# Kernel optimization log

Measured on AMD Instinct MI355X. Metric: run time of the kernel, lower is better.

Reference implementation:

```python
import jax, jax.numpy as jnp
import numpy as np

N = 20000
E_RAND = 320000
NEG_SLOPE = 0.2


def setup_inputs() -> dict:
    key = jax.random.key(0)
    ks = jax.random.split(key, 10)
    x = jax.random.normal(ks[0], (N, 768), dtype=jnp.float32)
    src = jax.random.randint(ks[1], (E_RAND,), 0, N)
    dst = jax.random.randint(ks[2], (E_RAND,), 0, N)
    loop = jnp.arange(N)
    edge_index = jnp.stack([jnp.concatenate([src, loop]),
                            jnp.concatenate([dst, loop])])  # [2, 340000]
    s = 1.0 / np.sqrt(768.0)
    W1 = jax.random.normal(ks[3], (768, 768), dtype=jnp.float32) * s
    a_src1 = jax.random.normal(ks[4], (8, 96), dtype=jnp.float32) * 0.1
    a_dst1 = jax.random.normal(ks[5], (8, 96), dtype=jnp.float32) * 0.1
    b1 = jnp.zeros((768,), dtype=jnp.float32)
    W2 = jax.random.normal(ks[6], (768, 768), dtype=jnp.float32) * s
    a_src2 = jax.random.normal(ks[7], (1, 768), dtype=jnp.float32) * 0.1
    a_dst2 = jax.random.normal(ks[8], (1, 768), dtype=jnp.float32) * 0.1
    b2 = jnp.zeros((768,), dtype=jnp.float32)
    return {"x": x, "edge_index": edge_index, "W1": W1, "a_src1": a_src1,
            "a_dst1": a_dst1, "b1": b1, "W2": W2, "a_src2": a_src2,
            "a_dst2": a_dst2, "b2": b2}


def gat_layer(x, W, a_src, a_dst, bias, src, dst, heads, out_c, concat):
    n = x.shape[0]
    h = (x @ W).reshape(n, heads, out_c)                      # [N,H,C]
    al_s = jnp.einsum('nhc,hc->nh', h, a_src)                 # [N,H]
    al_d = jnp.einsum('nhc,hc->nh', h, a_dst)
    e = jax.nn.leaky_relu(al_s[src] + al_d[dst], NEG_SLOPE)   # [E,H]
    m = jax.ops.segment_max(e, dst, num_segments=n)           # segment softmax
    ex = jnp.exp(e - m[dst])
    z = jax.ops.segment_sum(ex, dst, num_segments=n)
    alpha = ex / (z[dst] + 1e-16)                             # [E,H]
    msg = h[src] * alpha[:, :, None]                          # [E,H,C]
    out = jax.ops.segment_sum(msg, dst, num_segments=n)       # [N,H,C]
    out = out.reshape(n, heads * out_c) if concat else out.mean(axis=1)
    return out + bias


def reference(x, edge_index, W1, a_src1, a_dst1, b1, W2, a_src2, a_dst2, b2):
    src, dst = edge_index[0], edge_index[1]
    h = gat_layer(x, W1, a_src1, a_dst1, b1, src, dst, heads=8, out_c=96, concat=True)
    h = jax.nn.elu(h)
    out = gat_layer(h, W2, a_src2, a_dst2, b2, src, dst, heads=1, out_c=768, concat=False)
    return out
```

## Files before the change

kernel.cpp:

```cpp
#include <hip/hip_runtime.h>
#include <cstdint>
#include <cstddef>

typedef _Float16 f16;
typedef _Float16 f16x4 __attribute__((ext_vector_type(4)));
typedef _Float16 f16x8 __attribute__((ext_vector_type(8)));
typedef float f32x4 __attribute__((ext_vector_type(4)));

#define LRELU_SLOPE 0.2f

#define GLL16(g, l)                                                          \
  __builtin_amdgcn_global_load_lds(                                          \
      (const __attribute__((address_space(1))) void*)(g),                    \
      (__attribute__((address_space(3))) void*)(l), 16, 0, 0)

__global__ __launch_bounds__(256) void k_prep_xh(const float* __restrict__ x,
                                                 f16* __restrict__ xh,
                                                 int nvalid, int npad) {
  int total = npad * 192;
  for (int idx = blockIdx.x * blockDim.x + threadIdx.x; idx < total;
       idx += gridDim.x * blockDim.x) {
    int row = idx / 192;
    f16x4 o;
    if (row < nvalid) {
      const float4 v = *(const float4*)(x + (size_t)idx * 4);
      o[0] = (f16)v.x; o[1] = (f16)v.y; o[2] = (f16)v.z; o[3] = (f16)v.w;
    } else {
      o[0] = (f16)0.f; o[1] = (f16)0.f; o[2] = (f16)0.f; o[3] = (f16)0.f;
    }
    *(f16x4*)(xh + (size_t)idx * 4) = o;
  }
}

__global__ __launch_bounds__(256) void k_transpose_w(const float* __restrict__ W,
                                                     f16* __restrict__ Wt) {
  __shared__ float tile[32][33];
  int bn = blockIdx.x * 32;
  int bk = blockIdx.y * 32;
  int tx = threadIdx.x & 31, ty = threadIdx.x >> 5;
  #pragma unroll
  for (int r = ty; r < 32; r += 8)
    tile[r][tx] = W[(size_t)(bk + r) * 768 + bn + tx];
  __syncthreads();
  #pragma unroll
  for (int r = ty; r < 32; r += 8)
    Wt[(size_t)(bn + r) * 768 + bk + tx] = (f16)tile[tx][r];
}

__global__ void k_zero_ints(int* __restrict__ p, int n) {
  for (int i = blockIdx.x * blockDim.x + threadIdx.x; i < n;
       i += gridDim.x * blockDim.x) p[i] = 0;
}

__global__ void k_hist(const int* __restrict__ dst, int E, int* __restrict__ counts) {
  for (int e = blockIdx.x * blockDim.x + threadIdx.x; e < E;
       e += gridDim.x * blockDim.x) atomicAdd(&counts[dst[e]], 1);
}

__global__ __launch_bounds__(1024) void k_scan_block(const int* __restrict__ counts,
                                                     int* __restrict__ starts,
                                                     int* __restrict__ cursor, int n) {
  const int t = threadIdx.x;
  const int nthr = 1024;
  const int chunk = (n + nthr - 1) / nthr;
  const int base = t * chunk;
  int tsum = 0;
  for (int i = 0; i < chunk; i++) {
    int idx = base + i;
    if (idx < n) tsum += counts[idx];
  }
  int lane = t & 63, wv = t >> 6;
  int s = tsum;
  #pragma unroll
  for (int off = 1; off < 64; off <<= 1) {
    int tmp = __shfl_up(s, off);
    if (lane >= off) s += tmp;
  }
  __shared__ int wsum[16];
  if (lane == 63) wsum[wv] = s;
  __syncthreads();
  int woff = 0;
  for (int w = 0; w < wv; w++) woff += wsum[w];
  int run = woff + s - tsum;
  for (int i = 0; i < chunk; i++) {
    int idx = base + i;
    if (idx < n) {
      starts[idx] = run;
      cursor[idx] = run;
      run += counts[idx];
    }
  }
  if (t == nthr - 1) starts[n] = run;
}

__global__ void k_fill(const int* __restrict__ src, const int* __restrict__ dst, int E,
                       int* __restrict__ cursor, int* __restrict__ src_sorted) {
  for (int e = blockIdx.x * blockDim.x + threadIdx.x; e < E;
       e += gridDim.x * blockDim.x) {
    int slot = atomicAdd(&cursor[dst[e]], 1);
    src_sorted[slot] = src[e];
  }
}

__global__ __launch_bounds__(256) void k_gemm_f16(const f16* __restrict__ A,
                                                  const f16* __restrict__ Bt,
                                                  f16* __restrict__ C, int Mvalid) {
  __shared__ __align__(16) f16 As[4096];
  __shared__ __align__(16) f16 Bs[4096];
  const int K = 768;
  const int tid = threadIdx.x;
  const int bm = blockIdx.x * 128;
  const int bn = blockIdx.y * 128;
  const int lane = tid & 63;
  const int wave = tid >> 6;
  const int wr = (wave >> 1) * 64;
  const int wc = (wave & 1) * 64;

  const int r0 = tid >> 2;
  const int kc = (tid & 3) ^ ((r0 >> 1) & 3);
  const size_t offA0 = (size_t)(bm + r0) * K + kc * 8;
  const size_t offB0 = (size_t)(bn + r0) * K + kc * 8;
  f16* ldsA0 = As + wave * 512;
  f16* ldsA1 = As + 2048 + wave * 512;
  f16* ldsB0 = Bs + wave * 512;
  f16* ldsB1 = Bs + 2048 + wave * 512;

  f32x4 acc[4][4];
  const f32x4 vzero = {0.f, 0.f, 0.f, 0.f};
  #pragma unroll
  for (int i = 0; i < 4; i++)
    #pragma unroll
    for (int j = 0; j < 4; j++) acc[i][j] = vzero;

  const int fr = lane & 15;
  const int fq = lane >> 4;

  for (int k0 = 0; k0 < K; k0 += 32) {
    GLL16(A + offA0 + k0, ldsA0);
    GLL16(A + offA0 + (size_t)64 * K + k0, ldsA1);
    GLL16(Bt + offB0 + k0, ldsB0);
    GLL16(Bt + offB0 + (size_t)64 * K + k0, ldsB1);
    __syncthreads();
    f16x8 af[4], bf[4];
    #pragma unroll
    for (int i = 0; i < 4; i++) {
      const int r = wr + i * 16 + fr;
      const int slot = fq ^ ((r >> 1) & 3);
      af[i] = *(const f16x8*)(&As[r * 32 + slot * 8]);
    }
    #pragma unroll
    for (int j = 0; j < 4; j++) {
      const int r = wc + j * 16 + fr;
      const int slot = fq ^ ((r >> 1) & 3);
      bf[j] = *(const f16x8*)(&Bs[r * 32 + slot * 8]);
    }
    #pragma unroll
    for (int i = 0; i < 4; i++)
      #pragma unroll
      for (int j = 0; j < 4; j++)
        acc[i][j] = __builtin_amdgcn_mfma_f32_16x16x32_f16(af[i], bf[j], acc[i][j], 0, 0, 0);
    __syncthreads();
  }

  #pragma unroll
  for (int i = 0; i < 4; i++) {
    #pragma unroll
    for (int j = 0; j < 4; j++) {
      const int col = bn + wc + j * 16 + fr;
      #pragma unroll
      for (int r = 0; r < 4; r++) {
        const int row = bm + wr + i * 16 + fq * 4 + r;
        if (row < Mvalid) C[(size_t)row * 768 + col] = (f16)acc[i][j][r];
      }
    }
  }
}

template <int H>
__global__ __launch_bounds__(256) void k_al(const f16* __restrict__ h,
                                            const float* __restrict__ a_src,
                                            const float* __restrict__ a_dst,
                                            float* __restrict__ als,
                                            float* __restrict__ ald, int N) {
  int node = blockIdx.x * 4 + (threadIdx.x >> 6);
  int lane = threadIdx.x & 63;
  if (node >= N) return;
  const f16x4* hp = (const f16x4*)(h + (size_t)node * 768 + lane * 12);
  float ss = 0.f, sd = 0.f;
  int cbase = lane * 12;
  #pragma unroll
  for (int q = 0; q < 3; q++) {
    f16x4 hv = hp[q];
    #pragma unroll
    for (int j = 0; j < 4; j++) {
      int c = cbase + q * 4 + j;
      float v = (float)hv[j];
      ss += v * a_src[c];
      sd += v * a_dst[c];
    }
  }
  const int red = (H == 8) ? 8 : 64;
  #pragma unroll
  for (int off = 1; off < red; off <<= 1) {
    ss += __shfl_xor(ss, off);
    sd += __shfl_xor(sd, off);
  }
  if (H == 8) {
    if ((lane & 7) == 0) {
      als[(size_t)node * 8 + (lane >> 3)] = ss;
      ald[(size_t)node * 8 + (lane >> 3)] = sd;
    }
  } else {
    if (lane == 0) { als[node] = ss; ald[node] = sd; }
  }
}

template <int H, bool FINAL>
__global__ __launch_bounds__(192) void k_aggregate(
    const f16* __restrict__ h, const float* __restrict__ als,
    const float* __restrict__ ald, const int* __restrict__ starts,
    const int* __restrict__ src_sorted, const float* __restrict__ bias,
    void* __restrict__ outv, int nvalid) {
  const int n = blockIdx.x;
  const int t = threadIdx.x;
  if (n >= nvalid) return;
  __shared__ float s_ex[256 * H];
  __shared__ int s_src[256];
  __shared__ float s_zp[3][H];
  const int start = starts[n];
  const int deg = starts[n + 1] - start;
  const int lane = t & 63, wv = t >> 6;
  const int hA = (H == 8) ? (t & 7) : 0;
  const int myh = (H == 8) ? (t / 24) : 0;
  const float ald_A = ald[(size_t)n * H + hA];

  float zpart = 0.f;
  float4 acc = {0.f, 0.f, 0.f, 0.f};

  for (int cb = 0; cb < deg; cb += 256) {
    const int cnt = min(256, deg - cb);
    for (int idx = t; idx < cnt * H; idx += 192) {
      const int e = (H == 8) ? (idx >> 3) : idx;
      const int s = src_sorted[start + cb + e];
      if (H == 1 || (idx & 7) == 0) s_src[e] = s;
      float v = als[(size_t)s * H + hA] + ald_A;
      v = v > 0.f ? v : LRELU_SLOPE * v;
      const float ex = __expf(v);
      s_ex[idx] = ex;
      zpart += ex;
    }
    __syncthreads();
    for (int e = 0; e < cnt; e++) {
      const f16x4 hv = *(const f16x4*)(h + (size_t)s_src[e] * 768 + 4 * t);
      const float a = s_ex[e * H + myh];
      acc.x += a * (float)hv[0];
      acc.y += a * (float)hv[1];
      acc.z += a * (float)hv[2];
      acc.w += a * (float)hv[3];
    }
    __syncthreads();
  }

  if (H == 8) {
    #pragma unroll
    for (int off = 8; off < 64; off <<= 1) zpart += __shfl_xor(zpart, off);
    if (lane < 8) s_zp[wv][lane] = zpart;
  } else {
    #pragma unroll
    for (int off = 1; off < 64; off <<= 1) zpart += __shfl_xor(zpart, off);
    if (lane == 0) s_zp[wv][0] = zpart;
  }
  __syncthreads();
  const float z = s_zp[0][myh] + s_zp[1][myh] + s_zp[2][myh];
  const float inv = 1.f / (z + 1e-16f);

  const float4 bv = *(const float4*)(bias + 4 * t);
  float v0 = acc.x * inv + bv.x;
  float v1 = acc.y * inv + bv.y;
  float v2 = acc.z * inv + bv.z;
  float v3 = acc.w * inv + bv.w;
  if (!FINAL) {
    v0 = v0 > 0.f ? v0 : expm1f(v0);
    v1 = v1 > 0.f ? v1 : expm1f(v1);
    v2 = v2 > 0.f ? v2 : expm1f(v2);
    v3 = v3 > 0.f ? v3 : expm1f(v3);
    f16x4 o;
    o[0] = (f16)v0; o[1] = (f16)v1; o[2] = (f16)v2; o[3] = (f16)v3;
    *(f16x4*)((f16*)outv + (size_t)n * 768 + 4 * t) = o;
  } else {
    float4 o = {v0, v1, v2, v3};
    *(float4*)((float*)outv + (size_t)n * 768 + 4 * t) = o;
  }
}

extern "C" void kernel_launch(void* const* d_in, const int* in_sizes, int n_in,
                              void* d_out, int out_size, void* d_ws, size_t ws_size,
                              hipStream_t stream) {
  const float* x   = (const float*)d_in[0];
  const int*   ei  = (const int*)d_in[1];
  const float* W1  = (const float*)d_in[2];
  const float* as1 = (const float*)d_in[3];
  const float* ad1 = (const float*)d_in[4];
  const float* b1  = (const float*)d_in[5];
  const float* W2  = (const float*)d_in[6];
  const float* as2 = (const float*)d_in[7];
  const float* ad2 = (const float*)d_in[8];
  const float* b2  = (const float*)d_in[9];

  const int N = in_sizes[0] / 768;
  const int E = in_sizes[1] / 2;
  const int Mpad = (N + 127) & ~127;
  const int* srcp = ei;
  const int* dstp = ei + E;

  char* p = (char*)d_ws;
  auto alloc = [&](size_t b) { char* r = p; p += (b + 255) & ~(size_t)255; return r; };
  f16*   bufX   = (f16*)alloc((size_t)Mpad * 768 * sizeof(f16));
  f16*   bufH   = (f16*)alloc((size_t)Mpad * 768 * sizeof(f16));
  f16*   Wt1    = (f16*)alloc((size_t)768 * 768 * sizeof(f16));
  f16*   Wt2    = (f16*)alloc((size_t)768 * 768 * sizeof(f16));
  float* als1   = (float*)alloc((size_t)N * 8 * sizeof(float));
  float* ald1   = (float*)alloc((size_t)N * 8 * sizeof(float));
  float* als2   = (float*)alloc((size_t)N * sizeof(float));
  float* ald2   = (float*)alloc((size_t)N * sizeof(float));
  int*   counts = (int*)alloc((size_t)N * sizeof(int));
  int*   starts = (int*)alloc(((size_t)N + 1) * sizeof(int));
  int*   cursor = (int*)alloc((size_t)N * sizeof(int));
  int*   srcs   = (int*)alloc((size_t)E * sizeof(int));

  k_zero_ints<<<dim3(80), dim3(256), 0, stream>>>(counts, N);
  k_hist<<<dim3(512), dim3(256), 0, stream>>>(dstp, E, counts);
  k_scan_block<<<dim3(1), dim3(1024), 0, stream>>>(counts, starts, cursor, N);
  k_fill<<<dim3(512), dim3(256), 0, stream>>>(srcp, dstp, E, cursor, srcs);

  k_prep_xh<<<dim3(1024), dim3(256), 0, stream>>>(x, bufX, N, Mpad);
  k_transpose_w<<<dim3(24, 24), dim3(256), 0, stream>>>(W1, Wt1);
  k_transpose_w<<<dim3(24, 24), dim3(256), 0, stream>>>(W2, Wt2);

  k_gemm_f16<<<dim3(Mpad / 128, 6), dim3(256), 0, stream>>>(bufX, Wt1, bufH, N);
  k_al<8><<<dim3((N + 3) / 4), dim3(256), 0, stream>>>(bufH, as1, ad1, als1, ald1, N);
  k_aggregate<8, false><<<dim3(N), dim3(192), 0, stream>>>(bufH, als1, ald1, starts, srcs, b1, bufX, N);

  k_gemm_f16<<<dim3(Mpad / 128, 6), dim3(256), 0, stream>>>(bufX, Wt2, bufH, N);
  k_al<1><<<dim3((N + 3) / 4), dim3(256), 0, stream>>>(bufH, as2, ad2, als2, ald2, N);
  k_aggregate<1, true><<<dim3(N), dim3(192), 0, stream>>>(bufH, als2, ald2, starts, srcs, b2, d_out, N);
}
```

Baseline: 351.5 us.

## Slice h into 96-column planes and split aggregation per slice with precomputed edge weights

```diff
diff --git a/kernel.cpp b/kernel.cpp
--- a/kernel.cpp
+++ b/kernel.cpp
@@ -94,17 +94,20 @@
 }
 
 __global__ void k_fill(const int* __restrict__ src, const int* __restrict__ dst, int E,
-                       int* __restrict__ cursor, int* __restrict__ src_sorted) {
+                       int* __restrict__ cursor, int* __restrict__ src_sorted,
+                       int* __restrict__ dst_sorted) {
   for (int e = blockIdx.x * blockDim.x + threadIdx.x; e < E;
        e += gridDim.x * blockDim.x) {
     int slot = atomicAdd(&cursor[dst[e]], 1);
     src_sorted[slot] = src[e];
+    dst_sorted[slot] = dst[e];
   }
 }
 
 __global__ __launch_bounds__(256) void k_gemm_f16(const f16* __restrict__ A,
                                                   const f16* __restrict__ Bt,
-                                                  f16* __restrict__ C, int Mvalid) {
+                                                  f16* __restrict__ C, int Mvalid,
+                                                  int SS) {
   __shared__ __align__(16) f16 As[4096];
   __shared__ __align__(16) f16 Bs[4096];
   const int K = 768;
@@ -167,30 +170,34 @@
     #pragma unroll
     for (int j = 0; j < 4; j++) {
       const int col = bn + wc + j * 16 + fr;
+      const int cs = col / 96;
+      const int cw = col - cs * 96;
+      f16* cp = C + (size_t)cs * SS + cw;
       #pragma unroll
       for (int r = 0; r < 4; r++) {
         const int row = bm + wr + i * 16 + fq * 4 + r;
-        if (row < Mvalid) C[(size_t)row * 768 + col] = (f16)acc[i][j][r];
+        if (row < Mvalid) cp[(size_t)row * 96] = (f16)acc[i][j][r];
       }
     }
   }
 }
 
 template <int H>
-__global__ __launch_bounds__(256) void k_al(const f16* __restrict__ h,
+__global__ __launch_bounds__(256) void k_al(const f16* __restrict__ hs,
                                             const float* __restrict__ a_src,
                                             const float* __restrict__ a_dst,
                                             float* __restrict__ als,
-                                            float* __restrict__ ald, int N) {
+                                            float* __restrict__ ald, int N, int SS) {
   int node = blockIdx.x * 4 + (threadIdx.x >> 6);
   int lane = threadIdx.x & 63;
   if (node >= N) return;
-  const f16x4* hp = (const f16x4*)(h + (size_t)node * 768 + lane * 12);
+  const int sl = lane >> 3, wl = lane & 7;
+  const f16* hp = hs + (size_t)sl * SS + (size_t)node * 96 + wl * 12;
   float ss = 0.f, sd = 0.f;
-  int cbase = lane * 12;
+  const int cbase = sl * 96 + wl * 12;
   #pragma unroll
   for (int q = 0; q < 3; q++) {
-    f16x4 hv = hp[q];
+    f16x4 hv = *(const f16x4*)(hp + q * 4);
     #pragma unroll
     for (int j = 0; j < 4; j++) {
       int c = cbase + q * 4 + j;
@@ -207,89 +214,83 @@
   }
   if (H == 8) {
     if ((lane & 7) == 0) {
-      als[(size_t)node * 8 + (lane >> 3)] = ss;
-      ald[(size_t)node * 8 + (lane >> 3)] = sd;
+      als[(size_t)node * 8 + sl] = ss;
+      ald[(size_t)node * 8 + sl] = sd;
     }
   } else {
     if (lane == 0) { als[node] = ss; ald[node] = sd; }
   }
 }
 
+template <int H>
+__global__ __launch_bounds__(256) void k_alpha(const float* __restrict__ als,
+                                               const float* __restrict__ ald,
+                                               const int* __restrict__ srcs,
+                                               const int* __restrict__ dsts,
+                                               float* __restrict__ ex, int E) {
+  const int e = blockIdx.x * 256 + threadIdx.x;
+  if (e >= E) return;
+  const int s = srcs[e], d = dsts[e];
+  #pragma unroll
+  for (int h = 0; h < H; h++) {
+    float v = als[(size_t)s * H + h] + ald[(size_t)d * H + h];
+    v = v > 0.f ? v : LRELU_SLOPE * v;
+    ex[(size_t)h * E + e] = __expf(v);
+  }
+}
+
 template <int H, bool FINAL>
-__global__ __launch_bounds__(192) void k_aggregate(
-    const f16* __restrict__ h, const float* __restrict__ als,
-    const float* __restrict__ ald, const int* __restrict__ starts,
-    const int* __restrict__ src_sorted, const float* __restrict__ bias,
-    void* __restrict__ outv, int nvalid) {
-  const int n = blockIdx.x;
+__global__ __launch_bounds__(192) void k_agg2(
+    const f16* __restrict__ hs, const float* __restrict__ ex,
+    const int* __restrict__ starts, const int* __restrict__ srcs,
+    const float* __restrict__ bias, void* __restrict__ outv,
+    int N, int SS, int E) {
+  const int s = blockIdx.x & 7;
+  const int n = blockIdx.x >> 3;
   const int t = threadIdx.x;
-  if (n >= nvalid) return;
-  __shared__ float s_ex[256 * H];
-  __shared__ int s_src[256];
-  __shared__ float s_zp[3][H];
+  const int k = t / 24;
+  const int c = t - k * 24;
+  const int head = (H == 8) ? s : 0;
   const int start = starts[n];
   const int deg = starts[n + 1] - start;
-  const int lane = t & 63, wv = t >> 6;
-  const int hA = (H == 8) ? (t & 7) : 0;
-  const int myh = (H == 8) ? (t / 24) : 0;
-  const float ald_A = ald[(size_t)n * H + hA];
-
-  float zpart = 0.f;
+  const f16* hsl = hs + (size_t)s * SS;
+  const float* exp_ = ex + (size_t)head * E;
+
   float4 acc = {0.f, 0.f, 0.f, 0.f};
-
-  for (int cb = 0; cb < deg; cb += 256) {
-    const int cnt = min(256, deg - cb);
-    for (int idx = t; idx < cnt * H; idx += 192) {
-      const int e = (H == 8) ? (idx >> 3) : idx;
-      const int s = src_sorted[start + cb + e];
-      if (H == 1 || (idx & 7) == 0) s_src[e] = s;
-      float v = als[(size_t)s * H + hA] + ald_A;
-      v = v > 0.f ? v : LRELU_SLOPE * v;
-      const float ex = __expf(v);
-      s_ex[idx] = ex;
-      zpart += ex;
-    }
-    __syncthreads();
-    for (int e = 0; e < cnt; e++) {
-      const f16x4 hv = *(const f16x4*)(h + (size_t)s_src[e] * 768 + 4 * t);
-      const float a = s_ex[e * H + myh];
-      acc.x += a * (float)hv[0];
-      acc.y += a * (float)hv[1];
-      acc.z += a * (float)hv[2];
-      acc.w += a * (float)hv[3];
-    }
-    __syncthreads();
-  }
-
-  if (H == 8) {
-    #pragma unroll
-    for (int off = 8; off < 64; off <<= 1) zpart += __shfl_xor(zpart, off);
-    if (lane < 8) s_zp[wv][lane] = zpart;
-  } else {
-    #pragma unroll
-    for (int off = 1; off < 64; off <<= 1) zpart += __shfl_xor(zpart, off);
-    if (lane == 0) s_zp[wv][0] = zpart;
-  }
+  float z = 0.f;
+  for (int i = k; i < deg; i += 8) {
+    const int slot = start + i;
+    const float a = exp_[slot];
+    const int sv = srcs[slot];
+    const f16x4 hv = *(const f16x4*)(hsl + (size_t)sv * 96 + c * 4);
+    z += a;
+    acc.x += a * (float)hv[0];
+    acc.y += a * (float)hv[1];
+    acc.z += a * (float)hv[2];
+    acc.w += a * (float)hv[3];
+  }
+
+  __shared__ float s_acc[8][96];
+  __shared__ float s_z[8];
+  *(float4*)&s_acc[k][c * 4] = acc;
+  if (c == 0) s_z[k] = z;
   __syncthreads();
-  const float z = s_zp[0][myh] + s_zp[1][myh] + s_zp[2][myh];
-  const float inv = 1.f / (z + 1e-16f);
-
-  const float4 bv = *(const float4*)(bias + 4 * t);
-  float v0 = acc.x * inv + bv.x;
-  float v1 = acc.y * inv + bv.y;
-  float v2 = acc.z * inv + bv.z;
-  float v3 = acc.w * inv + bv.w;
-  if (!FINAL) {
-    v0 = v0 > 0.f ? v0 : expm1f(v0);
-    v1 = v1 > 0.f ? v1 : expm1f(v1);
-    v2 = v2 > 0.f ? v2 : expm1f(v2);
-    v3 = v3 > 0.f ? v3 : expm1f(v3);
-    f16x4 o;
-    o[0] = (f16)v0; o[1] = (f16)v1; o[2] = (f16)v2; o[3] = (f16)v3;
-    *(f16x4*)((f16*)outv + (size_t)n * 768 + 4 * t) = o;
-  } else {
-    float4 o = {v0, v1, v2, v3};
-    *(float4*)((float*)outv + (size_t)n * 768 + 4 * t) = o;
+
+  if (t < 96) {
+    float v = 0.f;
+    #pragma unroll
+    for (int kk = 0; kk < 8; kk++) v += s_acc[kk][t];
+    float zt = 0.f;
+    #pragma unroll
+    for (int kk = 0; kk < 8; kk++) zt += s_z[kk];
+    const float inv = 1.f / (zt + 1e-16f);
+    float o = v * inv + bias[s * 96 + t];
+    if (FINAL) {
+      ((float*)outv)[(size_t)n * 768 + s * 96 + t] = o;
+    } else {
+      o = o > 0.f ? o : expm1f(o);
+      ((f16*)outv)[(size_t)n * 768 + s * 96 + t] = (f16)o;
+    }
   }
 }
 
@@ -310,6 +311,7 @@
   const int N = in_sizes[0] / 768;
   const int E = in_sizes[1] / 2;
   const int Mpad = (N + 127) & ~127;
+  const int SS = Mpad * 96;
   const int* srcp = ei;
   const int* dstp = ei + E;
 
@@ -319,6 +321,7 @@
   f16*   bufH   = (f16*)alloc((size_t)Mpad * 768 * sizeof(f16));
   f16*   Wt1    = (f16*)alloc((size_t)768 * 768 * sizeof(f16));
   f16*   Wt2    = (f16*)alloc((size_t)768 * 768 * sizeof(f16));
+  float* ex     = (float*)alloc((size_t)8 * E * sizeof(float));
   float* als1   = (float*)alloc((size_t)N * 8 * sizeof(float));
   float* ald1   = (float*)alloc((size_t)N * 8 * sizeof(float));
   float* als2   = (float*)alloc((size_t)N * sizeof(float));
@@ -327,21 +330,28 @@
   int*   starts = (int*)alloc(((size_t)N + 1) * sizeof(int));
   int*   cursor = (int*)alloc((size_t)N * sizeof(int));
   int*   srcs   = (int*)alloc((size_t)E * sizeof(int));
+  int*   dsts   = (int*)alloc((size_t)E * sizeof(int));
 
   k_zero_ints<<<dim3(80), dim3(256), 0, stream>>>(counts, N);
   k_hist<<<dim3(512), dim3(256), 0, stream>>>(dstp, E, counts);
   k_scan_block<<<dim3(1), dim3(1024), 0, stream>>>(counts, starts, cursor, N);
-  k_fill<<<dim3(512), dim3(256), 0, stream>>>(srcp, dstp, E, cursor, srcs);
+  k_fill<<<dim3(512), dim3(256), 0, stream>>>(srcp, dstp, E, cursor, srcs, dsts);
 
   k_prep_xh<<<dim3(1024), dim3(256), 0, stream>>>(x, bufX, N, Mpad);
   k_transpose_w<<<dim3(24, 24), dim3(256), 0, stream>>>(W1, Wt1);
   k_transpose_w<<<dim3(24, 24), dim3(256), 0, stream>>>(W2, Wt2);
 
-  k_gemm_f16<<<dim3(Mpad / 128, 6), dim3(256), 0, stream>>>(bufX, Wt1, bufH, N);
-  k_al<8><<<dim3((N + 3) / 4), dim3(256), 0, stream>>>(bufH, as1, ad1, als1, ald1, N);
-  k_aggregate<8, false><<<dim3(N), dim3(192), 0, stream>>>(bufH, als1, ald1, starts, srcs, b1, bufX, N);
-
-  k_gemm_f16<<<dim3(Mpad / 128, 6), dim3(256), 0, stream>>>(bufX, Wt2, bufH, N);
-  k_al<1><<<dim3((N + 3) / 4), dim3(256), 0, stream>>>(bufH, as2, ad2, als2, ald2, N);
-  k_aggregate<1, true><<<dim3(N), dim3(192), 0, stream>>>(bufH, als2, ald2, starts, srcs, b2, d_out, N);
-}
+  const int eb = (E + 255) / 256;
+
+  k_gemm_f16<<<dim3(Mpad / 128, 6), dim3(256), 0, stream>>>(bufX, Wt1, bufH, N, SS);
+  k_al<8><<<dim3((N + 3) / 4), dim3(256), 0, stream>>>(bufH, as1, ad1, als1, ald1, N, SS);
+  k_alpha<8><<<dim3(eb), dim3(256), 0, stream>>>(als1, ald1, srcs, dsts, ex, E);
+  k_agg2<8, false><<<dim3(N * 8), dim3(192), 0, stream>>>(
+      bufH, ex, starts, srcs, b1, bufX, N, SS, E);
+
+  k_gemm_f16<<<dim3(Mpad / 128, 6), dim3(256), 0, stream>>>(bufX, Wt2, bufH, N, SS);
+  k_al<1><<<dim3((N + 3) / 4), dim3(256), 0, stream>>>(bufH, as2, ad2, als2, ald2, N, SS);
+  k_alpha<1><<<dim3(eb), dim3(256), 0, stream>>>(als2, ald2, srcs, dsts, ex, E);
+  k_agg2<1, true><<<dim3(N * 8), dim3(192), 0, stream>>>(
+      bufH, ex, starts, srcs, b2, d_out, N, SS, E);
+}
```

After: 504.3 us. +43.5%, slower.
